# Performance work log

Measured on AMD Instinct MI355X. Metric: run time of the kernel, lower is better.

The kernel has to match this reference:

```python
import jax, jax.numpy as jnp
import numpy as np

EMBED_DIM = 1024
NUM_HEADS = 16
PROJ_DIM = EMBED_DIM // NUM_HEADS


def setup_inputs() -> dict:
    key = jax.random.key(0)
    ks = jax.random.split(key, 9)
    s = 1.0 / np.sqrt(EMBED_DIM)
    inp = {
        "inputs": jax.random.normal(ks[0], (4, 2048, EMBED_DIM), dtype=jnp.float32),
        "Wq": jax.random.normal(ks[1], (EMBED_DIM, EMBED_DIM), dtype=jnp.float32) * s,
        "bq": jnp.zeros((EMBED_DIM,), jnp.float32),
        "Wk": jax.random.normal(ks[2], (EMBED_DIM, EMBED_DIM), dtype=jnp.float32) * s,
        "bk": jnp.zeros((EMBED_DIM,), jnp.float32),
        "Wv": jax.random.normal(ks[3], (EMBED_DIM, EMBED_DIM), dtype=jnp.float32) * s,
        "bv": jnp.zeros((EMBED_DIM,), jnp.float32),
        "Wo": jax.random.normal(ks[4], (EMBED_DIM, EMBED_DIM), dtype=jnp.float32) * s,
        "bo": jnp.zeros((EMBED_DIM,), jnp.float32),
    }
    return inp


def _split_heads(x):
    # [B, S, E] -> [B, H, S, D]
    b, s, _ = x.shape
    return x.reshape(b, s, NUM_HEADS, PROJ_DIM).transpose(0, 2, 1, 3)


def reference(inputs, Wq, bq, Wk, bk, Wv, bv, Wo, bo):
    q = _split_heads(inputs @ Wq + bq)
    k = _split_heads(inputs @ Wk + bk)
    v = _split_heads(inputs @ Wv + bv)
    scale = 1.0 / jnp.sqrt(jnp.asarray(PROJ_DIM, inputs.dtype))
    scores = jnp.einsum("bhqd,bhkd->bhqk", q, k) * scale  # [B,H,S,S]
    weights = jax.nn.softmax(scores, axis=-1)
    attn = jnp.einsum("bhqk,bhkd->bhqd", weights, v)
    b, h, s, d = attn.shape
    concat = attn.transpose(0, 2, 1, 3).reshape(b, s, h * d)
    return concat @ Wo + bo
```

## Files before the change

kernel.cpp:

```cpp
#include <hip/hip_runtime.h>
#include <math.h>

#define EMB 1024
#define SEQ 2048
#define BATCH 4
#define NH 16
#define HD 64
#define MTOT (BATCH * SEQ)

typedef _Float16 half_t;
typedef _Float16 half8 __attribute__((ext_vector_type(8)));
typedef __fp16 fp16x2 __attribute__((ext_vector_type(2)));
typedef float floatx4 __attribute__((ext_vector_type(4)));
typedef float floatx16 __attribute__((ext_vector_type(16)));

#if __has_builtin(__builtin_amdgcn_exp2f)
#define EXP2(x) __builtin_amdgcn_exp2f(x)
#else
#define EXP2(x) exp2f(x)
#endif

#define QSCALE 0.18033688f

#define GLOAD16(gsrc, ldst)                                                   \
  __builtin_amdgcn_global_load_lds(                                           \
      (__attribute__((address_space(1))) void*)(gsrc),                        \
      (__attribute__((address_space(3))) void*)(ldst), 16, 0, 0)

__device__ __forceinline__ unsigned pkh(float a, float b) {
  union { fp16x2 h; unsigned u; } c;
  c.h = __builtin_amdgcn_cvt_pkrtz(a, b);
  return c.u;
}

__global__ __launch_bounds__(256) void conv_all(const float* __restrict__ x,
                                                half_t* __restrict__ xh,
                                                const float* __restrict__ W0,
                                                const float* __restrict__ W1,
                                                const float* __restrict__ W2,
                                                const float* __restrict__ W3,
                                                half_t* __restrict__ wt) {
  __shared__ float T[64][68];
  const int bid = blockIdx.x;
  const int t = threadIdx.x;
  if (bid < 4096) {
    int i = bid * 256 + t;
    float4 a = ((const float4*)x)[i * 2];
    float4 b = ((const float4*)x)[i * 2 + 1];
    float v[8] = {a.x, a.y, a.z, a.w, b.x, b.y, b.z, b.w};
    half8 o;
#pragma unroll
    for (int j = 0; j < 8; ++j) o[j] = (half_t)v[j];
    *(half8*)(xh + (size_t)i * 8) = o;
    return;
  }
  const int b2 = bid - 4096;
  const int z = b2 >> 8, rem = b2 & 255;
  const int k0 = (rem >> 4) * 64, n0 = (rem & 15) * 64;
  const float* W = (z == 0) ? W0 : (z == 1) ? W1 : (z == 2) ? W2 : W3;
  half_t* wto = wt + (size_t)z * 1048576;
#pragma unroll
  for (int i = 0; i < 4; ++i) {
    int idx = t + i * 256;
    int row = idx >> 4, c4 = (idx & 15) << 2;
    *(float4*)(&T[row][c4]) = *(const float4*)(W + (size_t)(k0 + row) * EMB + n0 + c4);
  }
  __syncthreads();
#pragma unroll
  for (int cc = 0; cc < 2; ++cc) {
    int c = t + cc * 256;
    int n = c >> 3, g = c & 7;
    half8 hh;
#pragma unroll
    for (int j = 0; j < 8; ++j) hh[j] = (half_t)T[g * 8 + j][n];
    *(half8*)(wto + (size_t)(n0 + n) * EMB + k0 + g * 8) = hh;
  }
}

__global__ __launch_bounds__(256) void gemm_qkv(const half_t* __restrict__ A,
                                                const half_t* __restrict__ WT,
                                                const float* __restrict__ bq,
                                                const float* __restrict__ bk,
                                                const float* __restrict__ bvv,
                                                half_t* __restrict__ Qh,
                                                half_t* __restrict__ Kh,
                                                half_t* __restrict__ Vt) {
  __shared__ half_t lds[17536];
  half_t* As = lds;
  half_t* Bs = lds + 4096;

  const int mat = blockIdx.x;
  const half_t* B = WT + (size_t)mat * 1048576;
  const float* bias = (mat == 0) ? bq : (mat == 1) ? bk : bvv;
  const float scale = (mat == 0) ? QSCALE : 1.0f;
  half_t* outh = (mat == 0) ? Qh : (mat == 1) ? Kh : Vt;

  const int t = threadIdx.x;
  const int l = t & 63, w = t >> 6;
  const int wm = w >> 1, wn = w & 1;
  const int lr = l & 15, lg = l >> 4;
  const int row0 = blockIdx.y * 128, col0 = blockIdx.z * 128;

  const int sr2 = (w << 4) + (l >> 2);
  const int swz = (l & 3) ^ (sr2 & 3);
  const int rdsw = (lg ^ (lr & 3)) << 3;

  floatx4 acc[4][4];
#pragma unroll
  for (int i = 0; i < 4; ++i)
#pragma unroll
    for (int j = 0; j < 4; ++j) acc[i][j] = (floatx4){0.f, 0.f, 0.f, 0.f};

  for (int kb = 0; kb < EMB; kb += 32) {
    __syncthreads();
    GLOAD16(A + (size_t)(row0 + sr2) * EMB + kb + swz * 8, As + ((w << 4) << 5));
    GLOAD16(A + (size_t)(row0 + 64 + sr2) * EMB + kb + swz * 8,
            As + ((64 + (w << 4)) << 5));
    GLOAD16(B + (size_t)(col0 + sr2) * EMB + kb + swz * 8, Bs + ((w << 4) << 5));
    GLOAD16(B + (size_t)(col0 + 64 + sr2) * EMB + kb + swz * 8,
            Bs + ((64 + (w << 4)) << 5));
    __syncthreads();

    half8 fa[4];
#pragma unroll
    for (int mf = 0; mf < 4; ++mf)
      fa[mf] = *(const half8*)(As + ((wm * 64 + mf * 16 + lr) << 5) + rdsw);
#pragma unroll
    for (int nf = 0; nf < 4; ++nf) {
      half8 fb = *(const half8*)(Bs + ((wn * 64 + nf * 16 + lr) << 5) + rdsw);
#pragma unroll
      for (int mf = 0; mf < 4; ++mf)
        acc[mf][nf] = __builtin_amdgcn_mfma_f32_16x16x32_f16(fa[mf], fb, acc[mf][nf], 0, 0, 0);
    }
  }

  float bv[4];
#pragma unroll
  for (int nf = 0; nf < 4; ++nf) bv[nf] = bias[col0 + wn * 64 + nf * 16 + lr];

  if (mat < 2) {
#pragma unroll
    for (int mf = 0; mf < 4; ++mf)
#pragma unroll
      for (int nf = 0; nf < 4; ++nf)
#pragma unroll
        for (int r = 0; r < 4; ++r) {
          int row = row0 + wm * 64 + mf * 16 + lg * 4 + r;
          int col = col0 + wn * 64 + nf * 16 + lr;
          int bb = row >> 11, ss = row & (SEQ - 1);
          int hh = col >> 6, dd = col & (HD - 1);
          float f = (acc[mf][nf][r] + bv[nf]) * scale;
          outh[((size_t)(bb * NH + hh) * SEQ + ss) * HD + dd] = (half_t)f;
        }
  } else {
    half_t* T = lds;
    const int bb = row0 >> 11, s0 = row0 & (SEQ - 1);
    __syncthreads();
#pragma unroll
    for (int mf = 0; mf < 4; ++mf)
#pragma unroll
      for (int nf = 0; nf < 4; ++nf)
#pragma unroll
        for (int r = 0; r < 4; ++r) {
          float f = acc[mf][nf][r] + bv[nf];
          T[(wm * 64 + mf * 16 + lg * 4 + r) * 137 + wn * 64 + nf * 16 + lr] = (half_t)f;
        }
    __syncthreads();
#pragma unroll
    for (int i = 0; i < 8; ++i) {
      int idx = t + i * 256;
      int n = idx >> 4, mg = idx & 15;
      int col = col0 + n;
      int hh = col >> 6, dd = col & (HD - 1);
      half8 pk;
#pragma unroll
      for (int j = 0; j < 8; ++j) pk[j] = T[(mg * 8 + j) * 137 + n];
      *(half8*)(outh + ((size_t)(bb * NH + hh) * HD + dd) * SEQ + s0 + mg * 8) = pk;
    }
  }
}

__global__ __launch_bounds__(256) void gemmo(const half_t* __restrict__ A,
                                             const half_t* __restrict__ B,
                                             const float* __restrict__ bias,
                                             float* __restrict__ outf) {
  __shared__ half_t lds[8192];
  half_t* As = lds;
  half_t* Bs = lds + 4096;

  const int t = threadIdx.x;
  const int l = t & 63, w = t >> 6;
  const int wm = w >> 1, wn = w & 1;
  const int lr = l & 15, lg = l >> 4;
  const int row0 = blockIdx.x * 128, col0 = blockIdx.y * 128;
  const int sr2 = (w << 4) + (l >> 2);
  const int swz = (l & 3) ^ (sr2 & 3);
  const int rdsw = (lg ^ (lr & 3)) << 3;

  floatx4 acc[4][4];
#pragma unroll
  for (int i = 0; i < 4; ++i)
#pragma unroll
    for (int j = 0; j < 4; ++j) acc[i][j] = (floatx4){0.f, 0.f, 0.f, 0.f};

  for (int kb = 0; kb < EMB; kb += 32) {
    __syncthreads();
    GLOAD16(A + (size_t)(row0 + sr2) * EMB + kb + swz * 8, As + ((w << 4) << 5));
    GLOAD16(A + (size_t)(row0 + 64 + sr2) * EMB + kb + swz * 8,
            As + ((64 + (w << 4)) << 5));
    GLOAD16(B + (size_t)(col0 + sr2) * EMB + kb + swz * 8, Bs + ((w << 4) << 5));
    GLOAD16(B + (size_t)(col0 + 64 + sr2) * EMB + kb + swz * 8,
            Bs + ((64 + (w << 4)) << 5));
    __syncthreads();

    half8 fa[4];
#pragma unroll
    for (int mf = 0; mf < 4; ++mf)
      fa[mf] = *(const half8*)(As + ((wm * 64 + mf * 16 + lr) << 5) + rdsw);
#pragma unroll
    for (int nf = 0; nf < 4; ++nf) {
      half8 fb = *(const half8*)(Bs + ((wn * 64 + nf * 16 + lr) << 5) + rdsw);
#pragma unroll
      for (int mf = 0; mf < 4; ++mf)
        acc[mf][nf] = __builtin_amdgcn_mfma_f32_16x16x32_f16(fa[mf], fb, acc[mf][nf], 0, 0, 0);
    }
  }

  float bv[4];
#pragma unroll
  for (int nf = 0; nf < 4; ++nf) bv[nf] = bias[col0 + wn * 64 + nf * 16 + lr];
#pragma unroll
  for (int mf = 0; mf < 4; ++mf)
#pragma unroll
    for (int nf = 0; nf < 4; ++nf)
#pragma unroll
      for (int r = 0; r < 4; ++r) {
        int row = row0 + wm * 64 + mf * 16 + lg * 4 + r;
        int col = col0 + wn * 64 + nf * 16 + lr;
        outf[(size_t)row * EMB + col] = acc[mf][nf][r] + bv[nf];
      }
}

__global__ __launch_bounds__(512) void attnh(const half_t* __restrict__ Q,
                                             const half_t* __restrict__ K,
                                             const half_t* __restrict__ Vt,
                                             half_t* __restrict__ att) {
  __shared__ half_t lds[2 * 4608];
  half_t* Ks = lds;
  half_t* Vs = lds + 4608;

  const int t = threadIdx.x, l = t & 63, wq = t >> 6;
  const int lq = l & 31, hi = l >> 5;
  const int hi8 = hi * 8, hi4 = hi * 4;
  const int bh = blockIdx.x;
  const int q0 = blockIdx.y * 256;
  const size_t kbase = (size_t)bh * SEQ * HD;
  const size_t vbase = (size_t)bh * HD * SEQ;
  const int srow = t >> 3, sg = t & 7;

  half8 qf[4];
  const int qrow = q0 + wq * 32 + lq;
#pragma unroll
  for (int s = 0; s < 4; ++s)
    qf[s] = *(const half8*)(Q + kbase + (size_t)qrow * HD + s * 16 + hi8);

  floatx16 o0, o1;
#pragma unroll
  for (int r = 0; r < 16; ++r) { o0[r] = 0.f; o1[r] = 0.f; }
  float l_s = 0.f;

  half8 kh_r = *(const half8*)(K + kbase + (size_t)srow * HD + sg * 8);
  half8 vh_r = *(const half8*)(Vt + vbase + (size_t)srow * SEQ + sg * 8);

  for (int kv = 0; kv < SEQ; kv += 64) {
    __syncthreads();
    *(half8*)(Ks + srow * 72 + sg * 8) = kh_r;
    *(half8*)(Vs + srow * 72 + sg * 8) = vh_r;
    __syncthreads();

    {
      int nk = (kv + 64) & (SEQ - 1);
      kh_r = *(const half8*)(K + kbase + (size_t)(nk + srow) * HD + sg * 8);
      vh_r = *(const half8*)(Vt + vbase + (size_t)srow * SEQ + nk + sg * 8);
    }

    floatx16 s0v, s1v;
#pragma unroll
    for (int r = 0; r < 16; ++r) { s0v[r] = 0.f; s1v[r] = 0.f; }
    __builtin_amdgcn_s_setprio(1);
#pragma unroll
    for (int s = 0; s < 4; ++s) {
      const int off = s * 16 + hi8;
      half8 kf0 = *(const half8*)(Ks + lq * 72 + off);
      half8 kf1 = *(const half8*)(Ks + (32 + lq) * 72 + off);
      s0v = __builtin_amdgcn_mfma_f32_32x32x16_f16(kf0, qf[s], s0v, 0, 0, 0);
      s1v = __builtin_amdgcn_mfma_f32_32x32x16_f16(kf1, qf[s], s1v, 0, 0, 0);
    }
    __builtin_amdgcn_s_setprio(0);

    float rsum = 0.f;
#pragma unroll
    for (int r = 0; r < 16; ++r) { s0v[r] = EXP2(s0v[r]); rsum += s0v[r]; }
#pragma unroll
    for (int r = 0; r < 16; ++r) { s1v[r] = EXP2(s1v[r]); rsum += s1v[r]; }
    rsum += __shfl_xor(rsum, 32);
    l_s += rsum;

#define PV_STEP(SC, RH, S)                                                    \
  {                                                                           \
    unsigned u0 = pkh(SC[(RH) * 8 + 0], SC[(RH) * 8 + 1]);                    \
    unsigned u1 = pkh(SC[(RH) * 8 + 2], SC[(RH) * 8 + 3]);                    \
    unsigned u2 = pkh(SC[(RH) * 8 + 4], SC[(RH) * 8 + 5]);                    \
    unsigned u3 = pkh(SC[(RH) * 8 + 6], SC[(RH) * 8 + 7]);                    \
    asm volatile("v_permlane32_swap_b32 %0, %1" : "+v"(u0), "+v"(u2));        \
    asm volatile("v_permlane32_swap_b32 %0, %1" : "+v"(u1), "+v"(u3));        \
    int4 pi = make_int4((int)u0, (int)u1, (int)u2, (int)u3);                  \
    half8 pa = *(half8*)&pi;                                                  \
    half8 vb0 = *(const half8*)(Vs + lq * 72 + (S) * 16 + hi8);               \
    half8 vb1 = *(const half8*)(Vs + (32 + lq) * 72 + (S) * 16 + hi8);        \
    __builtin_amdgcn_s_setprio(1);                                            \
    o0 = __builtin_amdgcn_mfma_f32_32x32x16_f16(pa, vb0, o0, 0, 0, 0);        \
    o1 = __builtin_amdgcn_mfma_f32_32x32x16_f16(pa, vb1, o1, 0, 0, 0);        \
    __builtin_amdgcn_s_setprio(0);                                            \
  }
    PV_STEP(s0v, 0, 0)
    PV_STEP(s0v, 1, 1)
    PV_STEP(s1v, 0, 2)
    PV_STEP(s1v, 1, 3)
#undef PV_STEP
  }

  float inv = 1.f / l_s;
  float il[16];
#pragma unroll
  for (int r = 0; r < 16; ++r)
    il[r] = __shfl(inv, ((r & 3) + 8 * (r >> 2)) + hi4);
  const int bb2 = bh >> 4, hh2 = bh & 15;
#pragma unroll
  for (int dblk = 0; dblk < 2; ++dblk)
#pragma unroll
    for (int r = 0; r < 16; ++r) {
      float f = (dblk ? o1[r] : o0[r]) * il[r];
      int qg = q0 + wq * 32 + ((r & 3) + 8 * (r >> 2)) + hi4;
      size_t off = ((size_t)bb2 * SEQ + qg) * EMB + hh2 * HD + dblk * 32 + lq;
      att[off] = (half_t)f;
    }
}

extern "C" void kernel_launch(void* const* d_in, const int* in_sizes, int n_in,
                              void* d_out, int out_size, void* d_ws, size_t ws_size,
                              hipStream_t stream) {
  const float* X  = (const float*)d_in[0];
  const float* Wq = (const float*)d_in[1];
  const float* bq = (const float*)d_in[2];
  const float* Wk = (const float*)d_in[3];
  const float* bk = (const float*)d_in[4];
  const float* Wv = (const float*)d_in[5];
  const float* bv = (const float*)d_in[6];
  const float* Wo = (const float*)d_in[7];
  const float* bo = (const float*)d_in[8];
  float* out = (float*)d_out;

  char* wsb = (char*)d_ws;
  const size_t MB = 1024 * 1024;
  half_t* Xh = (half_t*)(wsb);
  half_t* WT = (half_t*)(wsb + 17 * MB);
  half_t* Qh = (half_t*)(wsb + 26 * MB);
  half_t* Kh = (half_t*)(wsb + 43 * MB);
  half_t* Vt = (half_t*)d_out;
  half_t* att = Xh;

  half_t* WTq = WT;
  half_t* WTo = WT + 3145728;

  conv_all<<<dim3(5120), 256, 0, stream>>>(X, Xh, Wq, Wk, Wv, Wo, WT);

  gemm_qkv<<<dim3(3, MTOT / 128, EMB / 128), 256, 0, stream>>>(
      Xh, WTq, bq, bk, bv, Qh, Kh, Vt);

  attnh<<<dim3(BATCH * NH, SEQ / 256), 512, 0, stream>>>(Qh, Kh, Vt, att);

  gemmo<<<dim3(MTOT / 128, EMB / 128), 256, 0, stream>>>(att, WTo, bo, out);
}
```

Baseline: 195.3 us.

## Double-buffer K/V LDS tiles and compute softmax row sums via MFMA

The attention kernel now ping-pongs between two LDS buffers for K and V tiles. The next tile is written while the current one is consumed, which cuts the two barriers per iteration to one. The per-row exp sum is no longer a scalar reduction with a cross-lane shuffle; it is accumulated by an extra MFMA against a vector of ones, so row sums land in the same layout as the output accumulator. This removes the final shuffle-based normalization. In exchange it doubles LDS use, which may hurt occupancy, adds a third MFMA per PV step, and accumulates the row sums from fp16-rounded probabilities.

Result: no change. 198.3 us (+1.5%).

```diff
diff --git a/kernel.cpp b/kernel.cpp
--- a/kernel.cpp
+++ b/kernel.cpp
@@ -245,18 +245,17 @@
                                              const half_t* __restrict__ K,
                                              const half_t* __restrict__ Vt,
                                              half_t* __restrict__ att) {
-  __shared__ half_t lds[2 * 4608];
-  half_t* Ks = lds;
-  half_t* Vs = lds + 4608;
+  __shared__ half_t lds[4 * 4608];
 
   const int t = threadIdx.x, l = t & 63, wq = t >> 6;
   const int lq = l & 31, hi = l >> 5;
-  const int hi8 = hi * 8, hi4 = hi * 4;
+  const int hi8 = hi * 8;
   const int bh = blockIdx.x;
   const int q0 = blockIdx.y * 256;
   const size_t kbase = (size_t)bh * SEQ * HD;
   const size_t vbase = (size_t)bh * HD * SEQ;
   const int srow = t >> 3, sg = t & 7;
+  const int soff = srow * 72 + sg * 8;
 
   half8 qf[4];
   const int qrow = q0 + wq * 32 + lq;
@@ -264,22 +263,34 @@
   for (int s = 0; s < 4; ++s)
     qf[s] = *(const half8*)(Q + kbase + (size_t)qrow * HD + s * 16 + hi8);
 
-  floatx16 o0, o1;
-#pragma unroll
-  for (int r = 0; r < 16; ++r) { o0[r] = 0.f; o1[r] = 0.f; }
-  float l_s = 0.f;
+  half8 vone;
+#pragma unroll
+  for (int j = 0; j < 8; ++j) vone[j] = (half_t)1.0f;
+
+  floatx16 o0, o1, lsacc;
+#pragma unroll
+  for (int r = 0; r < 16; ++r) { o0[r] = 0.f; o1[r] = 0.f; lsacc[r] = 0.f; }
 
   half8 kh_r = *(const half8*)(K + kbase + (size_t)srow * HD + sg * 8);
   half8 vh_r = *(const half8*)(Vt + vbase + (size_t)srow * SEQ + sg * 8);
-
-  for (int kv = 0; kv < SEQ; kv += 64) {
-    __syncthreads();
-    *(half8*)(Ks + srow * 72 + sg * 8) = kh_r;
-    *(half8*)(Vs + srow * 72 + sg * 8) = vh_r;
-    __syncthreads();
+  *(half8*)(lds + soff) = kh_r;
+  *(half8*)(lds + 4608 + soff) = vh_r;
+  kh_r = *(const half8*)(K + kbase + (size_t)(64 + srow) * HD + sg * 8);
+  vh_r = *(const half8*)(Vt + vbase + (size_t)srow * SEQ + 64 + sg * 8);
+  __syncthreads();
+
+  for (int it = 0; it < SEQ / 64; ++it) {
+    const int cur = it & 1;
+    half_t* Kb = lds + (cur ? 9216 : 0);
+    half_t* Vb = Kb + 4608;
+    half_t* Kw = lds + (cur ? 0 : 9216);
+    half_t* Vw = Kw + 4608;
+
+    *(half8*)(Kw + soff) = kh_r;
+    *(half8*)(Vw + soff) = vh_r;
 
     {
-      int nk = (kv + 64) & (SEQ - 1);
+      int nk = ((it + 2) * 64) & (SEQ - 1);
       kh_r = *(const half8*)(K + kbase + (size_t)(nk + srow) * HD + sg * 8);
       vh_r = *(const half8*)(Vt + vbase + (size_t)srow * SEQ + nk + sg * 8);
     }
@@ -291,20 +302,17 @@
 #pragma unroll
     for (int s = 0; s < 4; ++s) {
       const int off = s * 16 + hi8;
-      half8 kf0 = *(const half8*)(Ks + lq * 72 + off);
-      half8 kf1 = *(const half8*)(Ks + (32 + lq) * 72 + off);
+      half8 kf0 = *(const half8*)(Kb + lq * 72 + off);
+      half8 kf1 = *(const half8*)(Kb + (32 + lq) * 72 + off);
       s0v = __builtin_amdgcn_mfma_f32_32x32x16_f16(kf0, qf[s], s0v, 0, 0, 0);
       s1v = __builtin_amdgcn_mfma_f32_32x32x16_f16(kf1, qf[s], s1v, 0, 0, 0);
     }
     __builtin_amdgcn_s_setprio(0);
 
-    float rsum = 0.f;
-#pragma unroll
-    for (int r = 0; r < 16; ++r) { s0v[r] = EXP2(s0v[r]); rsum += s0v[r]; }
-#pragma unroll
-    for (int r = 0; r < 16; ++r) { s1v[r] = EXP2(s1v[r]); rsum += s1v[r]; }
-    rsum += __shfl_xor(rsum, 32);
-    l_s += rsum;
+#pragma unroll
+    for (int r = 0; r < 16; ++r) s0v[r] = EXP2(s0v[r]);
+#pragma unroll
+    for (int r = 0; r < 16; ++r) s1v[r] = EXP2(s1v[r]);
 
 #define PV_STEP(SC, RH, S)                                                    \
   {                                                                           \
@@ -316,11 +324,12 @@
     asm volatile("v_permlane32_swap_b32 %0, %1" : "+v"(u1), "+v"(u3));        \
     int4 pi = make_int4((int)u0, (int)u1, (int)u2, (int)u3);                  \
     half8 pa = *(half8*)&pi;                                                  \
-    half8 vb0 = *(const half8*)(Vs + lq * 72 + (S) * 16 + hi8);               \
-    half8 vb1 = *(const half8*)(Vs + (32 + lq) * 72 + (S) * 16 + hi8);        \
+    half8 vb0 = *(const half8*)(Vb + lq * 72 + (S) * 16 + hi8);               \
+    half8 vb1 = *(const half8*)(Vb + (32 + lq) * 72 + (S) * 16 + hi8);        \
     __builtin_amdgcn_s_setprio(1);                                            \
     o0 = __builtin_amdgcn_mfma_f32_32x32x16_f16(pa, vb0, o0, 0, 0, 0);        \
     o1 = __builtin_amdgcn_mfma_f32_32x32x16_f16(pa, vb1, o1, 0, 0, 0);        \
+    lsacc = __builtin_amdgcn_mfma_f32_32x32x16_f16(pa, vone, lsacc, 0, 0, 0); \
     __builtin_amdgcn_s_setprio(0);                                            \
   }
     PV_STEP(s0v, 0, 0)
@@ -328,23 +337,20 @@
     PV_STEP(s1v, 0, 2)
     PV_STEP(s1v, 1, 3)
 #undef PV_STEP
-  }
-
-  float inv = 1.f / l_s;
-  float il[16];
-#pragma unroll
-  for (int r = 0; r < 16; ++r)
-    il[r] = __shfl(inv, ((r & 3) + 8 * (r >> 2)) + hi4);
+
+    __syncthreads();
+  }
+
+  const int hi4 = hi * 4;
   const int bb2 = bh >> 4, hh2 = bh & 15;
 #pragma unroll
-  for (int dblk = 0; dblk < 2; ++dblk)
-#pragma unroll
-    for (int r = 0; r < 16; ++r) {
-      float f = (dblk ? o1[r] : o0[r]) * il[r];
-      int qg = q0 + wq * 32 + ((r & 3) + 8 * (r >> 2)) + hi4;
-      size_t off = ((size_t)bb2 * SEQ + qg) * EMB + hh2 * HD + dblk * 32 + lq;
-      att[off] = (half_t)f;
-    }
+  for (int r = 0; r < 16; ++r) {
+    float il = 1.f / lsacc[r];
+    int qg = q0 + wq * 32 + ((r & 3) + 8 * (r >> 2)) + hi4;
+    size_t off = ((size_t)bb2 * SEQ + qg) * EMB + hh2 * HD + lq;
+    att[off] = (half_t)(o0[r] * il);
+    att[off + 32] = (half_t)(o1[r] * il);
+  }
 }
 
 extern "C" void kernel_launch(void* const* d_in, const int* in_sizes, int n_in,
```
